# Optimization experiments

Measured on AMD Instinct MI355X. Metric: run time of the kernel, lower is better.

The kernel has to match this reference:

```python
import jax, jax.numpy as jnp
import numpy as np

M, K, N, GROUP = 32, 8192, 28672, 128


def setup_inputs() -> dict:
    key = jax.random.key(0)
    k1, k2, k3, k4 = jax.random.split(key, 4)
    x = jax.random.normal(k1, (M, K), dtype=jnp.float16)
    # int32 words, each packing 8 consecutive int4 values along K
    qweight = jax.random.randint(k2, (K // 8, N), 0, 2147483647, dtype=jnp.int32)
    scales = (jax.random.uniform(k3, (K // GROUP, N), dtype=jnp.float32) * 0.01 + 0.001).astype(jnp.float16)
    bias = (jax.random.normal(k4, (N,), dtype=jnp.float32) * 0.02).astype(jnp.float16)
    return {"x": x, "qweight": qweight, "scales": scales, "bias": bias}


def reference(x, qweight, scales, bias):
    # Unpack 8 int4 nibbles per int32 word along K: (K//8, N) -> (K, N)
    K8, n = qweight.shape
    shifts = (jnp.arange(8, dtype=jnp.int32) * 4)[None, :, None]
    wq = ((qweight[:, None, :] >> shifts) & 15).reshape(K8 * 8, n)  # [K, N] in [0,15]
    # Dequant: zero-point fixed at 8 (pack() asserts zeros==8), per-group scales
    w = wq.astype(jnp.float16) - jnp.float16(8.0)
    g, gs = scales.shape[0], (K8 * 8) // scales.shape[0]
    w = (w.reshape(g, gs, n) * scales[:, None, :]).reshape(K8 * 8, n)  # [K, N] fp16
    return jnp.dot(x, w) + bias  # [M, N]
```

## Files before the change

kernel.cpp:

```cpp
#include <hip/hip_runtime.h>
#include <stdint.h>

#define K_DIM 8192
#define N_DIM 28672
#define NG    8

typedef _Float16 half8 __attribute__((ext_vector_type(8)));
typedef _Float16 half2t __attribute__((ext_vector_type(2)));
typedef float f32x16 __attribute__((ext_vector_type(16)));
typedef float f32x4 __attribute__((ext_vector_type(4)));
typedef uint32_t u32x4 __attribute__((ext_vector_type(4)));

__global__ __launch_bounds__(256) void prep_x(const float* __restrict__ x,
                                              _Float16* __restrict__ xp) {
  int idx = blockIdx.x * 256 + threadIdx.x;
  int m  = idx & 31;
  int k8 = idx >> 5;
  const float* p = x + (size_t)m * K_DIM + (size_t)k8 * 8;
  float4 xa = *(const float4*)p;
  float4 xb = *(const float4*)(p + 4);
  half2t p0 = __builtin_bit_cast(half2t, __builtin_amdgcn_cvt_pkrtz(xa.x, xb.x));
  half2t p1 = __builtin_bit_cast(half2t, __builtin_amdgcn_cvt_pkrtz(xa.y, xb.y));
  half2t p2 = __builtin_bit_cast(half2t, __builtin_amdgcn_cvt_pkrtz(xa.z, xb.z));
  half2t p3 = __builtin_bit_cast(half2t, __builtin_amdgcn_cvt_pkrtz(xa.w, xb.w));
  half8 o;
  o[0] = p0[0]; o[1] = p0[1]; o[2] = p1[0]; o[3] = p1[1];
  o[4] = p2[0]; o[5] = p2[1]; o[6] = p3[0]; o[7] = p3[1];
  *(half8*)(xp + ((size_t)k8 * 32 + m) * 8) = o;
}

static __device__ __forceinline__ half8 dqs(uint32_t w, half2t sh) {
  const uint32_t M4 = 0x000F000Fu, E = 0x64006400u;
  half2t off; off[0] = (_Float16)(-1032.0f); off[1] = (_Float16)(-1032.0f);
  half2t v0 = (__builtin_bit_cast(half2t, ( w        & M4) | E) + off) * sh;
  half2t v1 = (__builtin_bit_cast(half2t, ((w >> 4)  & M4) | E) + off) * sh;
  half2t v2 = (__builtin_bit_cast(half2t, ((w >> 8)  & M4) | E) + off) * sh;
  half2t v3 = (__builtin_bit_cast(half2t, ((w >> 12) & M4) | E) + off) * sh;
  half8 r;
  r[0] = v0[0]; r[1] = v0[1]; r[2] = v1[0]; r[3] = v1[1];
  r[4] = v2[0]; r[5] = v2[1]; r[6] = v3[0]; r[7] = v3[1];
  return r;
}

static __device__ __forceinline__ half2t cvtp(float f) {
  return __builtin_bit_cast(half2t, __builtin_amdgcn_cvt_pkrtz(f, f));
}

static __device__ __forceinline__ void waitcnt_vm8() { __builtin_amdgcn_s_waitcnt(0x0F78); }
static __device__ __forceinline__ void waitcnt_vm0() { __builtin_amdgcn_s_waitcnt(0x0F70); }

__global__ __launch_bounds__(512, 2) void qgemm(
    const uint32_t* __restrict__ q, const float* __restrict__ scales,
    const float* __restrict__ bias, const _Float16* __restrict__ xp,
    float* __restrict__ out) {
  __shared__ float red[8][16][64];
  const int tid  = threadIdx.x;
  const int w    = tid >> 6;
  const int lane = tid & 63;
  const int h    = lane >> 5;
  const int nl   = lane & 31;
  const int c0   = blockIdx.x << 7;
  const int wr0  = w << 7;

  half2t sh[8][4];
#pragma unroll
  for (int g = 0; g < NG; g++) {
    f32x4 sv = *(const f32x4*)&scales[(size_t)(w * NG + g) * N_DIM + c0 + 4 * nl];
    sh[g][0] = cvtp(sv[0]); sh[g][1] = cvtp(sv[1]);
    sh[g][2] = cvtp(sv[2]); sh[g][3] = cvtp(sv[3]);
  }
  waitcnt_vm0();
  __builtin_amdgcn_sched_barrier(0);

  const uint32_t qb = (uint32_t)((((uint64_t)(wr0 + h)) * N_DIM + c0 + 4 * nl) * 4);
  const uint32_t ab = (uint32_t)(((wr0 + h) * 32 + nl) * 16);

  u32x4 qr[2][8];
  f32x4 aA[8];

  auto qload = [&](int g, int p) {
#pragma unroll
    for (int i = 0; i < 8; i++) {
      uint32_t vo = qb + (uint32_t)(g * 16 + 2 * i) * (uint32_t)(N_DIM * 4);
      asm volatile("global_load_dwordx4 %0, %1, %2"
                   : "=v"(qr[p][i]) : "v"(vo), "s"(q));
    }
  };
  auto aload1 = [&](int g, int i) {
    uint32_t vo = ab + (uint32_t)(g * 8192 + i * 1024);
    asm volatile("global_load_dwordx4 %0, %1, %2"
                 : "=v"(aA[i]) : "v"(vo), "s"(xp));
  };

  f32x16 acc0, acc1, acc2, acc3;
#pragma unroll
  for (int j = 0; j < 16; j++) { acc0[j] = 0.f; acc1[j] = 0.f; acc2[j] = 0.f; acc3[j] = 0.f; }

  qload(0, 0);
#pragma unroll
  for (int i = 0; i < 8; i++) aload1(0, i);
  qload(1, 1);

#pragma unroll
  for (int g = 0; g < NG; g++) {
    if (g < NG - 1) waitcnt_vm8(); else waitcnt_vm0();
    __builtin_amdgcn_sched_barrier(0);
    half2t s0 = sh[g][0], s1 = sh[g][1], s2 = sh[g][2], s3 = sh[g][3];
#pragma unroll
    for (int i = 0; i < 8; i++) {
      half8 af = __builtin_bit_cast(half8, aA[i]);
      u32x4 qw = qr[g & 1][i];
      acc0 = __builtin_amdgcn_mfma_f32_32x32x16_f16(af, dqs(qw[0], s0), acc0, 0, 0, 0);
      acc1 = __builtin_amdgcn_mfma_f32_32x32x16_f16(af, dqs(qw[1], s1), acc1, 0, 0, 0);
      acc2 = __builtin_amdgcn_mfma_f32_32x32x16_f16(af, dqs(qw[2], s2), acc2, 0, 0, 0);
      acc3 = __builtin_amdgcn_mfma_f32_32x32x16_f16(af, dqs(qw[3], s3), acc3, 0, 0, 0);
      if (g + 1 < NG) aload1(g + 1, i);
    }
    if (g + 2 < NG) qload(g + 2, g & 1);
  }

#pragma unroll
  for (int J = 0; J < 4; J++) {
    f32x16 accJ = (J == 0) ? acc0 : (J == 1) ? acc1 : (J == 2) ? acc2 : acc3;
#pragma unroll
    for (int r = 0; r < 16; r++) red[w][r][lane] = accJ[r];
    __syncthreads();
#pragma unroll
    for (int s = 0; s < 2; s++) {
      int p   = tid + s * 512;
      int reg = p >> 6, ln = p & 63;
      float v = 0.f;
#pragma unroll
      for (int u = 0; u < 8; u++) v += red[u][reg][ln];
      int row = (reg & 3) + ((reg >> 2) << 3) + ((ln >> 5) << 2);
      int col = c0 + 4 * (ln & 31) + J;
      out[(size_t)row * N_DIM + col] = v + bias[col];
    }
    __syncthreads();
  }
}

extern "C" void kernel_launch(void* const* d_in, const int* in_sizes, int n_in,
                              void* d_out, int out_size, void* d_ws, size_t ws_size,
                              hipStream_t stream) {
  const float*    xf      = (const float*)d_in[0];
  const uint32_t* qweight = (const uint32_t*)d_in[1];
  const float*    scales  = (const float*)d_in[2];
  const float*    bias    = (const float*)d_in[3];
  float*          out     = (float*)d_out;
  _Float16*       xp      = (_Float16*)d_ws;

  prep_x<<<dim3(128), dim3(256), 0, stream>>>(xf, xp);
  qgemm<<<dim3(N_DIM / 128), dim3(512), 0, stream>>>(qweight, scales, bias, xp, out);
}
```

Measured before the change: 188.5 us.

## Split K across two blocks with atomic reduction and wider 256-column tiles

```diff
diff --git a/kernel.cpp b/kernel.cpp
--- a/kernel.cpp
+++ b/kernel.cpp
@@ -3,7 +3,6 @@
 
 #define K_DIM 8192
 #define N_DIM 28672
-#define NG    8
 
 typedef _Float16 half8 __attribute__((ext_vector_type(8)));
 typedef _Float16 half2t __attribute__((ext_vector_type(2)));
@@ -29,6 +28,10 @@
   *(half8*)(xp + ((size_t)k8 * 32 + m) * 8) = o;
 }
 
+__global__ __launch_bounds__(256) void zero_out(float4* __restrict__ out) {
+  out[(size_t)blockIdx.x * 256 + threadIdx.x] = float4{0.f, 0.f, 0.f, 0.f};
+}
+
 static __device__ __forceinline__ half8 dqs(uint32_t w, half2t sh) {
   const uint32_t M4 = 0x000F000Fu, E = 0x64006400u;
   half2t off; off[0] = (_Float16)(-1032.0f); off[1] = (_Float16)(-1032.0f);
@@ -46,8 +49,10 @@
   return __builtin_bit_cast(half2t, __builtin_amdgcn_cvt_pkrtz(f, f));
 }
 
-static __device__ __forceinline__ void waitcnt_vm8() { __builtin_amdgcn_s_waitcnt(0x0F78); }
-static __device__ __forceinline__ void waitcnt_vm0() { __builtin_amdgcn_s_waitcnt(0x0F70); }
+static __device__ __forceinline__ void wvm9() { __builtin_amdgcn_s_waitcnt(0x0F79); }
+static __device__ __forceinline__ void wvm6() { __builtin_amdgcn_s_waitcnt(0x0F76); }
+static __device__ __forceinline__ void wvm3() { __builtin_amdgcn_s_waitcnt(0x0F73); }
+static __device__ __forceinline__ void wvm0() { __builtin_amdgcn_s_waitcnt(0x0F70); }
 
 __global__ __launch_bounds__(512, 2) void qgemm(
     const uint32_t* __restrict__ q, const float* __restrict__ scales,
@@ -57,71 +62,88 @@
   const int tid  = threadIdx.x;
   const int w    = tid >> 6;
   const int lane = tid & 63;
-  const int h    = lane >> 5;
   const int nl   = lane & 31;
-  const int c0   = blockIdx.x << 7;
-  const int wr0  = w << 7;
+  const int bid  = blockIdx.x;
+  const int kb   = bid / 112;
+  const int ct   = bid - kb * 112;
+  const int c0   = ct << 8;
+  const int r0w  = (kb << 9) + (w << 6);
 
-  half2t sh[8][4];
+  half2t sh[4][8];
 #pragma unroll
-  for (int g = 0; g < NG; g++) {
-    f32x4 sv = *(const f32x4*)&scales[(size_t)(w * NG + g) * N_DIM + c0 + 4 * nl];
-    sh[g][0] = cvtp(sv[0]); sh[g][1] = cvtp(sv[1]);
-    sh[g][2] = cvtp(sv[2]); sh[g][3] = cvtp(sv[3]);
+  for (int gg = 0; gg < 4; gg++) {
+    int sg = (kb << 5) + (w << 2) + gg;
+    f32x4 sa = *(const f32x4*)&scales[(size_t)sg * N_DIM + c0 + 4 * nl];
+    f32x4 sb = *(const f32x4*)&scales[(size_t)sg * N_DIM + c0 + 128 + 4 * nl];
+    sh[gg][0] = cvtp(sa[0]); sh[gg][1] = cvtp(sa[1]);
+    sh[gg][2] = cvtp(sa[2]); sh[gg][3] = cvtp(sa[3]);
+    sh[gg][4] = cvtp(sb[0]); sh[gg][5] = cvtp(sb[1]);
+    sh[gg][6] = cvtp(sb[2]); sh[gg][7] = cvtp(sb[3]);
   }
-  waitcnt_vm0();
+  wvm0();
   __builtin_amdgcn_sched_barrier(0);
 
-  const uint32_t qb = (uint32_t)((((uint64_t)(wr0 + h)) * N_DIM + c0 + 4 * nl) * 4);
-  const uint32_t ab = (uint32_t)(((wr0 + h) * 32 + nl) * 16);
+  const uint32_t RS = (uint32_t)(N_DIM * 4);
+  const uint32_t qbase = (uint32_t)(((uint64_t)r0w * N_DIM + c0 + 4 * lane) * 4);
+  const int h = lane >> 5;
+  const uint32_t abase = (uint32_t)(((r0w + h) * 32 + nl) * 16);
 
-  u32x4 qr[2][8];
-  f32x4 aA[8];
+  u32x4 qa[4], qb4[4];
+  f32x4 aA[4];
 
-  auto qload = [&](int g, int p) {
-#pragma unroll
-    for (int i = 0; i < 8; i++) {
-      uint32_t vo = qb + (uint32_t)(g * 16 + 2 * i) * (uint32_t)(N_DIM * 4);
-      asm volatile("global_load_dwordx4 %0, %1, %2"
-                   : "=v"(qr[p][i]) : "v"(vo), "s"(q));
-    }
-  };
-  auto aload1 = [&](int g, int i) {
-    uint32_t vo = ab + (uint32_t)(g * 8192 + i * 1024);
+  auto issue = [&](int s) {
+    uint32_t va = qbase + (uint32_t)(2 * s) * RS;
     asm volatile("global_load_dwordx4 %0, %1, %2"
-                 : "=v"(aA[i]) : "v"(vo), "s"(xp));
+                 : "=v"(qa[s & 3]) : "v"(va), "s"(q));
+    asm volatile("global_load_dwordx4 %0, %1, %2"
+                 : "=v"(qb4[s & 3]) : "v"(va + RS), "s"(q));
+    uint32_t vA = abase + (uint32_t)(2 * s) * 512;
+    asm volatile("global_load_dwordx4 %0, %1, %2"
+                 : "=v"(aA[s & 3]) : "v"(vA), "s"(xp));
   };
 
-  f32x16 acc0, acc1, acc2, acc3;
+  f32x16 acc0, acc1, acc2, acc3, acc4, acc5, acc6, acc7;
 #pragma unroll
-  for (int j = 0; j < 16; j++) { acc0[j] = 0.f; acc1[j] = 0.f; acc2[j] = 0.f; acc3[j] = 0.f; }
+  for (int j = 0; j < 16; j++) {
+    acc0[j] = 0.f; acc1[j] = 0.f; acc2[j] = 0.f; acc3[j] = 0.f;
+    acc4[j] = 0.f; acc5[j] = 0.f; acc6[j] = 0.f; acc7[j] = 0.f;
+  }
 
-  qload(0, 0);
-#pragma unroll
-  for (int i = 0; i < 8; i++) aload1(0, i);
-  qload(1, 1);
+  issue(0); issue(1); issue(2); issue(3);
+
+#define SUB(J_, ACCL_, ACCH_)                                                 \
+  do {                                                                        \
+    uint32_t lo = qa[t][J_], hi = qb4[t][J_];                                 \
+    asm volatile("v_permlane32_swap_b32 %0, %1" : "+v"(lo), "+v"(hi));        \
+    ACCL_ = __builtin_amdgcn_mfma_f32_32x32x16_f16(af, dqs(lo, sh[gg][J_]),   \
+                                                   ACCL_, 0, 0, 0);           \
+    ACCH_ = __builtin_amdgcn_mfma_f32_32x32x16_f16(af, dqs(hi, sh[gg][J_+4]), \
+                                                   ACCH_, 0, 0, 0);           \
+  } while (0)
 
 #pragma unroll
-  for (int g = 0; g < NG; g++) {
-    if (g < NG - 1) waitcnt_vm8(); else waitcnt_vm0();
+  for (int s = 0; s < 32; ++s) {
+    if (s <= 27) wvm9();
+    else if (s == 28) wvm9();
+    else if (s == 29) wvm6();
+    else if (s == 30) wvm3();
+    else wvm0();
     __builtin_amdgcn_sched_barrier(0);
-    half2t s0 = sh[g][0], s1 = sh[g][1], s2 = sh[g][2], s3 = sh[g][3];
-#pragma unroll
-    for (int i = 0; i < 8; i++) {
-      half8 af = __builtin_bit_cast(half8, aA[i]);
-      u32x4 qw = qr[g & 1][i];
-      acc0 = __builtin_amdgcn_mfma_f32_32x32x16_f16(af, dqs(qw[0], s0), acc0, 0, 0, 0);
-      acc1 = __builtin_amdgcn_mfma_f32_32x32x16_f16(af, dqs(qw[1], s1), acc1, 0, 0, 0);
-      acc2 = __builtin_amdgcn_mfma_f32_32x32x16_f16(af, dqs(qw[2], s2), acc2, 0, 0, 0);
-      acc3 = __builtin_amdgcn_mfma_f32_32x32x16_f16(af, dqs(qw[3], s3), acc3, 0, 0, 0);
-      if (g + 1 < NG) aload1(g + 1, i);
-    }
-    if (g + 2 < NG) qload(g + 2, g & 1);
+    const int t = s & 3, gg = s >> 3;
+    half8 af = __builtin_bit_cast(half8, aA[t]);
+    SUB(0, acc0, acc4);
+    SUB(1, acc1, acc5);
+    SUB(2, acc2, acc6);
+    SUB(3, acc3, acc7);
+    if (s + 4 < 32) issue(s + 4);
   }
+#undef SUB
 
 #pragma unroll
-  for (int J = 0; J < 4; J++) {
-    f32x16 accJ = (J == 0) ? acc0 : (J == 1) ? acc1 : (J == 2) ? acc2 : acc3;
+  for (int J = 0; J < 8; J++) {
+    f32x16 accJ = (J == 0) ? acc0 : (J == 1) ? acc1 : (J == 2) ? acc2 :
+                  (J == 3) ? acc3 : (J == 4) ? acc4 : (J == 5) ? acc5 :
+                  (J == 6) ? acc6 : acc7;
 #pragma unroll
     for (int r = 0; r < 16; r++) red[w][r][lane] = accJ[r];
     __syncthreads();
@@ -133,8 +155,9 @@
 #pragma unroll
       for (int u = 0; u < 8; u++) v += red[u][reg][ln];
       int row = (reg & 3) + ((reg >> 2) << 3) + ((ln >> 5) << 2);
-      int col = c0 + 4 * (ln & 31) + J;
-      out[(size_t)row * N_DIM + col] = v + bias[col];
+      int col = c0 + ((J >> 2) << 7) + 4 * (ln & 31) + (J & 3);
+      float add = v + ((kb == 0) ? bias[col] : 0.f);
+      unsafeAtomicAdd(&out[(size_t)row * N_DIM + col], add);
     }
     __syncthreads();
   }
@@ -150,6 +173,7 @@
   float*          out     = (float*)d_out;
   _Float16*       xp      = (_Float16*)d_ws;
 
+  zero_out<<<dim3(896), dim3(256), 0, stream>>>((float4*)out);
   prep_x<<<dim3(128), dim3(256), 0, stream>>>(xf, xp);
-  qgemm<<<dim3(N_DIM / 128), dim3(512), 0, stream>>>(qweight, scales, bias, xp, out);
+  qgemm<<<dim3(224), dim3(512), 0, stream>>>(qweight, scales, bias, xp, out);
 }
```

Measured after the change: 202.7 us. 7.6% more time.
